# Kernel tuning notes

Hardware: AMD Instinct MI355X
Metric: run time of the kernel (lower is better)

## Reference

```python
import jax, jax.numpy as jnp
import numpy as np

BN_EPS = 1e-5

def _square_distance(src, dst):
    # src: (B,N,3), dst: (B,S,3) -> (B,N,S)
    d = -2.0 * jnp.einsum('bnc,bsc->bns', src, dst)
    d = d + jnp.sum(src * src, -1)[:, :, None]
    d = d + jnp.sum(dst * dst, -1)[:, None, :]
    return d

def _bn_relu(x, gamma, beta):
    # x: (B,N,C); training-mode batchnorm over (B,N)
    mean = jnp.mean(x, axis=(0, 1))
    var = jnp.mean(jnp.square(x - mean), axis=(0, 1))
    y = (x - mean) * jax.lax.rsqrt(var + BN_EPS) * gamma + beta
    return jax.nn.relu(y)

def setup_inputs() -> dict:
    key = jax.random.key(0)
    ks = jax.random.split(key, 12)
    B, N, S, D1, D2 = 8, 8192, 2048, 128, 256
    in_ch, mlp = 384, [256, 256]
    inp = {
        'xyz1': jax.random.normal(ks[0], (B, 3, N), jnp.float32),
        'xyz2': jax.random.normal(ks[1], (B, 3, S), jnp.float32),
        'points1': jax.random.normal(ks[2], (B, D1, N), jnp.float32),
        'points2': jax.random.normal(ks[3], (B, D2, S), jnp.float32),
    }
    last = in_ch
    for i, out in enumerate(mlp):
        inp[f'W{i+1}'] = jax.random.normal(ks[4 + 2 * i], (out, last), jnp.float32) * (1.0 / np.sqrt(last))
        inp[f'b{i+1}'] = jnp.zeros((out,), jnp.float32)
        inp[f'g{i+1}'] = jnp.ones((out,), jnp.float32)
        inp[f'beta{i+1}'] = jnp.zeros((out,), jnp.float32)
        last = out
    return inp

def reference(xyz1, xyz2, points1, points2, W1, b1, g1, beta1, W2, b2, g2, beta2):
    p1 = jnp.transpose(xyz1, (0, 2, 1))   # (B,N,3)
    p2 = jnp.transpose(xyz2, (0, 2, 1))   # (B,S,3)
    f2 = jnp.transpose(points2, (0, 2, 1))  # (B,S,D2)

    dists = _square_distance(p1, p2)      # (B,N,S)
    neg_d, idx = jax.lax.top_k(-dists, 3)  # 3 smallest distances
    d3 = -neg_d                            # (B,N,3)
    dist_recip = 1.0 / (d3 + 1e-8)
    weight = dist_recip / jnp.sum(dist_recip, axis=2, keepdims=True)  # (B,N,3)

    gathered = jax.vmap(lambda p, i: p[i])(f2, idx)   # (B,N,3,D2)
    interp = jnp.sum(gathered * weight[..., None], axis=2)  # (B,N,D2)

    f1 = jnp.transpose(points1, (0, 2, 1))  # (B,N,D1)
    x = jnp.concatenate([f1, interp], axis=-1)  # (B,N,D1+D2)

    x = _bn_relu(jnp.einsum('bnc,oc->bno', x, W1) + b1, g1, beta1)
    x = _bn_relu(jnp.einsum('bnc,oc->bno', x, W2) + b2, g2, beta2)
    return jnp.transpose(x, (0, 2, 1))  # (B,256,N)
```

## Files before the change

### kernel.cpp

```cpp
#include <hip/hip_runtime.h>

#define B_   8
#define N_   8192
#define S_   2048
#define D1_  128
#define D2_  256
#define O_   256
#define BN_  (B_*N_)

typedef __bf16 bf16;
typedef __bf16 bf16x8_t __attribute__((ext_vector_type(8)));
typedef __bf16 bf16x4_t __attribute__((ext_vector_type(4)));
typedef float  f32x4_t  __attribute__((ext_vector_type(4)));

static const size_t OFF_IDX  = 0;
static const size_t OFF_W    = 786432;
static const size_t OFF_PRT  = 393216;
static const size_t OFF_XP   = 1572864;
static const size_t OFF_Z    = 51904512;
static const size_t OFF_SS1  = 85458944;
static const size_t OFF_SS2  = 85460992;

#define GL16(gsrc, ldst) \
  __builtin_amdgcn_global_load_lds((const __attribute__((address_space(1))) void*)(gsrc), \
                                   (__attribute__((address_space(3))) void*)(ldst), 16, 0, 0)

__global__ __launch_bounds__(256) void k_prep(const float* __restrict__ p1, bf16* __restrict__ xp,
                                              const float* __restrict__ p2, bf16* __restrict__ f2t) {
  __shared__ float lds[64][65];
  const int bid = blockIdx.x;
  const int t = threadIdx.x;
  if (bid < 1024) {
    const int g  = bid * 256 + t;
    const int n4 = g & 2047;
    const int c8 = (g >> 11) & 15;
    const int b  = g >> 15;
    const int n  = n4 * 4;
    const float* src = p1 + ((size_t)b * D1_ + c8 * 8) * N_ + n;
    bf16x8_t o0, o1, o2, o3;
    #pragma unroll
    for (int j = 0; j < 8; ++j) {
      float4 v = *(const float4*)(src + (size_t)j * N_);
      o0[j] = (bf16)v.x; o1[j] = (bf16)v.y; o2[j] = (bf16)v.z; o3[j] = (bf16)v.w;
    }
    bf16* dst = xp + (((size_t)b * 48 + c8) * N_ + n) * 8;
    *(bf16x8_t*)(dst)      = o0;
    *(bf16x8_t*)(dst + 8)  = o1;
    *(bf16x8_t*)(dst + 16) = o2;
    *(bf16x8_t*)(dst + 24) = o3;
  } else {
    const int bid2 = bid - 1024;
    const int b = bid2 & 7;
    const int inner = bid2 >> 3;
    const int s0 = (inner & 31) * 64;
    const int c0 = (inner >> 5) * 64;
    {
      const int cr = t >> 2, scb = (t & 3) * 16;
      const float* src = p2 + ((size_t)b * D2_ + c0 + cr) * S_ + s0 + scb;
      #pragma unroll
      for (int i = 0; i < 4; ++i) {
        const float4 v = *(const float4*)(src + 4 * i);
        lds[cr][scb + 4 * i + 0] = v.x; lds[cr][scb + 4 * i + 1] = v.y;
        lds[cr][scb + 4 * i + 2] = v.z; lds[cr][scb + 4 * i + 3] = v.w;
      }
    }
    __syncthreads();
    const int co = (t & 7) * 8;
    #pragma unroll
    for (int pass = 0; pass < 2; ++pass) {
      const int s = pass * 32 + (t >> 3);
      bf16x8_t o;
      #pragma unroll
      for (int j = 0; j < 8; ++j) o[j] = (bf16)lds[co + j][s];
      *(bf16x8_t*)(f2t + ((size_t)b * S_ + s0 + s) * D2_ + c0 + co) = o;
    }
  }
}

__device__ __forceinline__ void ins3(float d, int i,
                                     float& d0, float& d1, float& d2,
                                     int& i0, int& i1, int& i2) {
  const bool c2 = d < d2, c1 = d < d1, c0 = d < d0;
  const float nd2 = c1 ? d1 : (c2 ? d : d2); const int ni2 = c1 ? i1 : (c2 ? i : i2);
  const float nd1 = c0 ? d0 : (c1 ? d : d1); const int ni1 = c0 ? i0 : (c1 ? i : i1);
  d0 = c0 ? d : d0; i0 = c0 ? i : i0;
  d1 = nd1; i1 = ni1; d2 = nd2; i2 = ni2;
}

__global__ __launch_bounds__(256) void k_nn3(const float* __restrict__ xyz1, const float* __restrict__ xyz2,
                                             int* __restrict__ idxw, float* __restrict__ www) {
  __shared__ float4 sq[4][S_ / 4];
  __shared__ float  pd[4][64][3];
  __shared__ int    pi[4][64][3];
  const int tid  = threadIdx.x;
  const int lane = tid & 63, w = tid >> 6;
  const int b     = blockIdx.y;
  const int nbase = blockIdx.x * 64;

  const float* x2 = xyz2 + (size_t)b * 3 * S_;
  for (int j = tid; j < S_ / 4; j += 256) {
    const float4 x = *(const float4*)(x2 + 4 * j);
    const float4 y = *(const float4*)(x2 + S_ + 4 * j);
    const float4 z = *(const float4*)(x2 + 2 * S_ + 4 * j);
    float4 qq;
    qq.x = fmaf(x.x, x.x, fmaf(y.x, y.x, z.x * z.x));
    qq.y = fmaf(x.y, x.y, fmaf(y.y, y.y, z.y * z.y));
    qq.z = fmaf(x.z, x.z, fmaf(y.z, y.z, z.z * z.z));
    qq.w = fmaf(x.w, x.w, fmaf(y.w, y.w, z.w * z.w));
    sq[0][j] = x; sq[1][j] = y; sq[2][j] = z; sq[3][j] = qq;
  }

  const int n = nbase + lane;
  const float* x1 = xyz1 + (size_t)b * 3 * N_;
  const float px = x1[n], py = x1[N_ + n], pz = x1[2 * N_ + n];
  const float ax = -2.f * px, ay = -2.f * py, az = -2.f * pz;
  __syncthreads();

  float e0 = 3.4e38f, e1 = 3.4e38f, e2 = 3.4e38f;
  int   i0 = 0, i1 = 0, i2 = 0;

  const int jb = w * (S_ / 16);
  #pragma unroll 2
  for (int j = jb; j < jb + S_ / 16; ++j) {
    const float4 qx = sq[0][j], qy = sq[1][j], qz = sq[2][j], qq = sq[3][j];
    #define CAND(C, SI)                                                        \
      {                                                                        \
        const float E = fmaf(ax, qx.C, fmaf(ay, qy.C, fmaf(az, qz.C, qq.C))); \
        if (__any(E < e2)) {                                                   \
          const bool l0 = E < e0, l1 = E < e1, l2 = E < e2;                    \
          const int ni1 = l0 ? i0 : (l1 ? (SI) : i1);                          \
          const int ni2 = l1 ? i1 : (l2 ? (SI) : i2);                          \
          i0 = l0 ? (SI) : i0; i1 = ni1; i2 = ni2;                             \
          const float ne1 = __builtin_amdgcn_fmed3f(E, e0, e1);                \
          const float ne2 = __builtin_amdgcn_fmed3f(E, e1, e2);                \
          e0 = fminf(E, e0); e1 = ne1; e2 = ne2;                               \
        }                                                                      \
      }
    CAND(x, 4 * j + 0)
    CAND(y, 4 * j + 1)
    CAND(z, 4 * j + 2)
    CAND(w, 4 * j + 3)
    #undef CAND
  }

  const float pp = fmaf(px, px, fmaf(py, py, pz * pz));
  pd[w][lane][0] = e0 + pp; pd[w][lane][1] = e1 + pp; pd[w][lane][2] = e2 + pp;
  pi[w][lane][0] = i0; pi[w][lane][1] = i1; pi[w][lane][2] = i2;
  __syncthreads();

  if (tid < 64) {
    float d0 = pd[0][tid][0], d1 = pd[0][tid][1], d2 = pd[0][tid][2];
    int   j0 = pi[0][tid][0], j1 = pi[0][tid][1], j2 = pi[0][tid][2];
    #pragma unroll
    for (int ck = 1; ck < 4; ++ck)
      #pragma unroll
      for (int k = 0; k < 3; ++k)
        ins3(pd[ck][tid][k], pi[ck][tid][k], d0, d1, d2, j0, j1, j2);
    const float r0 = 1.f / (d0 + 1e-8f), r1 = 1.f / (d1 + 1e-8f), r2 = 1.f / (d2 + 1e-8f);
    const float inv = 1.f / (r0 + r1 + r2);
    const int bn = b * N_ + nbase + tid;
    idxw[bn] = j0; idxw[BN_ + bn] = j1; idxw[2 * BN_ + bn] = j2;
    www[bn] = r0 * inv; www[BN_ + bn] = r1 * inv; www[2 * BN_ + bn] = r2 * inv;
  }
}

__global__ __launch_bounds__(256) void k_interp(const bf16* __restrict__ f2t, const int* __restrict__ idxw,
                                                const float* __restrict__ www, bf16* __restrict__ xp) {
  const int bid = blockIdx.x;
  const int b = bid & 7;
  const int n = (bid >> 3) * 8 + (threadIdx.x & 7);
  const int c8 = threadIdx.x >> 3;
  const int bn = b * N_ + n;
  const int j0 = idxw[bn], j1 = idxw[BN_ + bn], j2 = idxw[2 * BN_ + bn];
  const float w0 = www[bn], w1 = www[BN_ + bn], w2 = www[2 * BN_ + bn];
  const bf16* base = f2t + (size_t)b * S_ * D2_ + c8 * 8;
  const bf16x8_t v0 = *(const bf16x8_t*)(base + (size_t)j0 * D2_);
  const bf16x8_t v1 = *(const bf16x8_t*)(base + (size_t)j1 * D2_);
  const bf16x8_t v2 = *(const bf16x8_t*)(base + (size_t)j2 * D2_);
  bf16x8_t out;
  #pragma unroll
  for (int j = 0; j < 8; ++j)
    out[j] = (bf16)(w0 * (float)v0[j] + w1 * (float)v1[j] + w2 * (float)v2[j]);
  *(bf16x8_t*)(xp + (((size_t)b * 48 + 16 + c8) * N_ + (size_t)n) * 8) = out;
}

__global__ __launch_bounds__(256) void k_wprep(const float* __restrict__ W1, const float* __restrict__ W2,
                                               bf16* __restrict__ img) {
  const int g = blockIdx.x * 256 + threadIdx.x;
  if (g < 12288) {
    const int e = g * 8;
    const int imgblk = e >> 12, r = e & 4095;
    const int kc = r >> 10, row = (r & 1023) >> 3;
    const int mblk = imgblk / 12, kt32 = imgblk % 12;
    const float* s = W1 + (size_t)(mblk * 128 + row) * 384 + kt32 * 32 + kc * 8;
    const float4 f0 = *(const float4*)(s), f1 = *(const float4*)(s + 4);
    bf16x8_t h;
    h[0] = (bf16)f0.x; h[1] = (bf16)f0.y; h[2] = (bf16)f0.z; h[3] = (bf16)f0.w;
    h[4] = (bf16)f1.x; h[5] = (bf16)f1.y; h[6] = (bf16)f1.z; h[7] = (bf16)f1.w;
    *(bf16x8_t*)(img + e) = h;
  } else if (g < 20480) {
    const int e = (g - 12288) * 8;
    const int imgblk = e >> 12, r = e & 4095;
    const int kc = r >> 10, row = (r & 1023) >> 3;
    const int mblk = imgblk >> 3, kt32 = imgblk & 7;
    const float* s = W2 + (size_t)(mblk * 128 + row) * 256 + kt32 * 32 + kc * 8;
    const float4 f0 = *(const float4*)(s), f1 = *(const float4*)(s + 4);
    bf16x8_t h;
    h[0] = (bf16)f0.x; h[1] = (bf16)f0.y; h[2] = (bf16)f0.z; h[3] = (bf16)f0.w;
    h[4] = (bf16)f1.x; h[5] = (bf16)f1.y; h[6] = (bf16)f1.z; h[7] = (bf16)f1.w;
    *(bf16x8_t*)(img + 98304 + e) = h;
  }
}

template<int K>
__global__ __launch_bounds__(256) void k_gemm(const bf16* __restrict__ Wimg, const float* __restrict__ bias,
                                              const bf16* __restrict__ X, bf16* __restrict__ Zp,
                                              float* __restrict__ part) {
  __shared__ bf16 As[4096];
  __shared__ bf16 Bt[4096];
  __shared__ float stl[2][128][2];
  const int tid = threadIdx.x;
  const int lane = tid & 63, wid = tid >> 6;
  const int wr = wid >> 1, wc = wid & 1;
  const int dd = blockIdx.x;
  const int xcd = dd & 7, pos = dd >> 3;
  const int b = pos >> 4, q = pos & 15;
  const int m0 = (q & 1) * 128;
  const int ncol = xcd * 8 + (q >> 1);
  const int n0 = ncol * 128;
  const int mblk = m0 >> 7;
  const int l15 = lane & 15, l4 = lane >> 4;

  f32x4_t acc[4][4];
  #pragma unroll
  for (int i = 0; i < 4; ++i)
    #pragma unroll
    for (int j = 0; j < 4; ++j) { f32x4_t z = {0.f, 0.f, 0.f, 0.f}; acc[i][j] = z; }

  const bf16* Xb = X + (size_t)b * (K / 8) * ((size_t)N_ * 8);

  for (int kt = 0; kt < K; kt += 32) {
    const bf16* asrc = Wimg + (size_t)(mblk * (K / 32) + (kt >> 5)) * 4096 + wid * 1024 + lane * 8;
    GL16(asrc,       &As[wid * 1024]);
    GL16(asrc + 512, &As[wid * 1024 + 512]);
    const bf16* bsrc = Xb + ((size_t)(kt >> 3) + wid) * ((size_t)N_ * 8) + ((size_t)n0 + lane) * 8;
    GL16(bsrc,       &Bt[wid * 1024]);
    GL16(bsrc + 512, &Bt[wid * 1024 + 512]);
    __syncthreads();
    bf16x8_t af[4], bfr[4];
    #pragma unroll
    for (int mi = 0; mi < 4; ++mi) af[mi]  = *(const bf16x8_t*)&As[l4 * 1024 + (wr * 64 + mi * 16 + l15) * 8];
    #pragma unroll
    for (int ni = 0; ni < 4; ++ni) bfr[ni] = *(const bf16x8_t*)&Bt[l4 * 1024 + (wc * 64 + ni * 16 + l15) * 8];
    #pragma unroll
    for (int mi = 0; mi < 4; ++mi)
      #pragma unroll
      for (int ni = 0; ni < 4; ++ni)
        acc[mi][ni] = __builtin_amdgcn_mfma_f32_16x16x32_bf16(af[mi], bfr[ni], acc[mi][ni], 0, 0, 0);
    __syncthreads();
  }
  bf16* Zb = Zp + (size_t)b * 32 * ((size_t)N_ * 8);
  #pragma unroll
  for (int mi = 0; mi < 4; ++mi) {
    const int obase = m0 + wr * 64 + mi * 16 + l4 * 4;
    const float4 bv = *(const float4*)(bias + obase);
    const size_t gofs = (size_t)(obase >> 3) * ((size_t)N_ * 8) + (obase & 7);
    float sv0 = 0.f, sv1 = 0.f, sv2 = 0.f, sv3 = 0.f;
    float qv0 = 0.f, qv1 = 0.f, qv2 = 0.f, qv3 = 0.f;
    #pragma unroll
    for (int ni = 0; ni < 4; ++ni) {
      const int nn = n0 + wc * 64 + ni * 16 + l15;
      const float v0 = acc[mi][ni][0] + bv.x;
      const float v1 = acc[mi][ni][1] + bv.y;
      const float v2 = acc[mi][ni][2] + bv.z;
      const float v3 = acc[mi][ni][3] + bv.w;
      bf16x4_t o;
      o[0] = (bf16)v0; o[1] = (bf16)v1; o[2] = (bf16)v2; o[3] = (bf16)v3;
      *(bf16x4_t*)(Zb + gofs + (size_t)nn * 8) = o;
      sv0 += v0; qv0 = fmaf(v0, v0, qv0);
      sv1 += v1; qv1 = fmaf(v1, v1, qv1);
      sv2 += v2; qv2 = fmaf(v2, v2, qv2);
      sv3 += v3; qv3 = fmaf(v3, v3, qv3);
    }
    #pragma unroll
    for (int off = 1; off < 16; off <<= 1) {
      sv0 += __shfl_xor(sv0, off); qv0 += __shfl_xor(qv0, off);
      sv1 += __shfl_xor(sv1, off); qv1 += __shfl_xor(qv1, off);
      sv2 += __shfl_xor(sv2, off); qv2 += __shfl_xor(qv2, off);
      sv3 += __shfl_xor(sv3, off); qv3 += __shfl_xor(qv3, off);
    }
    if (l15 == 0) {
      const int ol = wr * 64 + mi * 16 + l4 * 4;
      stl[wc][ol + 0][0] = sv0; stl[wc][ol + 0][1] = qv0;
      stl[wc][ol + 1][0] = sv1; stl[wc][ol + 1][1] = qv1;
      stl[wc][ol + 2][0] = sv2; stl[wc][ol + 2][1] = qv2;
      stl[wc][ol + 3][0] = sv3; stl[wc][ol + 3][1] = qv3;
    }
  }
  __syncthreads();
  if (tid < 128) {
    const float s  = stl[0][tid][0] + stl[1][tid][0];
    const float sq = stl[0][tid][1] + stl[1][tid][1];
    const int ib = b * 64 + ncol;
    part[(size_t)(m0 + tid) * 512 + ib]       = s;
    part[(size_t)(256 + m0 + tid) * 512 + ib] = sq;
  }
}

__global__ __launch_bounds__(256) void k_gemm2f(const bf16* __restrict__ Wimg, const float* __restrict__ bias,
                                                const bf16* __restrict__ Z1, const float* __restrict__ ss,
                                                bf16* __restrict__ Zp, float* __restrict__ part) {
  __shared__ bf16 As[4096];
  __shared__ bf16 Bt[4096];
  __shared__ float stl[2][128][2];
  __shared__ float ssl[512];
  const int tid = threadIdx.x;
  const int lane = tid & 63, wid = tid >> 6;
  const int wr = wid >> 1, wc = wid & 1;
  const int dd = blockIdx.x;
  const int xcd = dd & 7, pos = dd >> 3;
  const int b = pos >> 4, q = pos & 15;
  const int m0 = (q & 1) * 128;
  const int ncol = xcd * 8 + (q >> 1);
  const int n0 = ncol * 128;
  const int mblk = m0 >> 7;
  const int l15 = lane & 15, l4 = lane >> 4;

  ssl[tid] = ss[tid]; ssl[256 + tid] = ss[256 + tid];

  f32x4_t acc[4][4];
  #pragma unroll
  for (int i = 0; i < 4; ++i)
    #pragma unroll
    for (int j = 0; j < 4; ++j) { f32x4_t z = {0.f, 0.f, 0.f, 0.f}; acc[i][j] = z; }

  const bf16* Z1b = Z1 + (size_t)b * 32 * ((size_t)N_ * 8);
  __syncthreads();

  for (int kt = 0; kt < 256; kt += 32) {
    const bf16* asrc = Wimg + (size_t)(mblk * 8 + (kt >> 5)) * 4096 + wid * 1024 + lane * 8;
    GL16(asrc,       &As[wid * 1024]);
    GL16(asrc + 512, &As[wid * 1024 + 512]);
    const int kc8 = (kt >> 3) + wid;
    const bf16* bsrc = Z1b + (size_t)kc8 * ((size_t)N_ * 8) + ((size_t)n0 + lane) * 8;
    const bf16x8_t rb0 = *(const bf16x8_t*)(bsrc);
    const bf16x8_t rb1 = *(const bf16x8_t*)(bsrc + 512);
    const int cb = kc8 * 8;
    bf16x8_t ob0, ob1;
    #pragma unroll
    for (int j = 0; j < 8; ++j) {
      const float sc = ssl[cb + j], sh = ssl[256 + cb + j];
      ob0[j] = (bf16)fmaxf(fmaf((float)rb0[j], sc, sh), 0.f);
      ob1[j] = (bf16)fmaxf(fmaf((float)rb1[j], sc, sh), 0.f);
    }
    *(bf16x8_t*)&Bt[wid * 1024 + lane * 8]       = ob0;
    *(bf16x8_t*)&Bt[wid * 1024 + 512 + lane * 8] = ob1;
    __syncthreads();
    bf16x8_t af[4], bfr[4];
    #pragma unroll
    for (int mi = 0; mi < 4; ++mi) af[mi]  = *(const bf16x8_t*)&As[l4 * 1024 + (wr * 64 + mi * 16 + l15) * 8];
    #pragma unroll
    for (int ni = 0; ni < 4; ++ni) bfr[ni] = *(const bf16x8_t*)&Bt[l4 * 1024 + (wc * 64 + ni * 16 + l15) * 8];
    #pragma unroll
    for (int mi = 0; mi < 4; ++mi)
      #pragma unroll
      for (int ni = 0; ni < 4; ++ni)
        acc[mi][ni] = __builtin_amdgcn_mfma_f32_16x16x32_bf16(af[mi], bfr[ni], acc[mi][ni], 0, 0, 0);
    __syncthreads();
  }
  bf16* Zb = Zp + (size_t)b * 32 * ((size_t)N_ * 8);
  #pragma unroll
  for (int mi = 0; mi < 4; ++mi) {
    const int obase = m0 + wr * 64 + mi * 16 + l4 * 4;
    const float4 bv = *(const float4*)(bias + obase);
    const size_t gofs = (size_t)(obase >> 3) * ((size_t)N_ * 8) + (obase & 7);
    float sv0 = 0.f, sv1 = 0.f, sv2 = 0.f, sv3 = 0.f;
    float qv0 = 0.f, qv1 = 0.f, qv2 = 0.f, qv3 = 0.f;
    #pragma unroll
    for (int ni = 0; ni < 4; ++ni) {
      const int nn = n0 + wc * 64 + ni * 16 + l15;
      const float v0 = acc[mi][ni][0] + bv.x;
      const float v1 = acc[mi][ni][1] + bv.y;
      const float v2 = acc[mi][ni][2] + bv.z;
      const float v3 = acc[mi][ni][3] + bv.w;
      bf16x4_t o;
      o[0] = (bf16)v0; o[1] = (bf16)v1; o[2] = (bf16)v2; o[3] = (bf16)v3;
      *(bf16x4_t*)(Zb + gofs + (size_t)nn * 8) = o;
      sv0 += v0; qv0 = fmaf(v0, v0, qv0);
      sv1 += v1; qv1 = fmaf(v1, v1, qv1);
      sv2 += v2; qv2 = fmaf(v2, v2, qv2);
      sv3 += v3; qv3 = fmaf(v3, v3, qv3);
    }
    #pragma unroll
    for (int off = 1; off < 16; off <<= 1) {
      sv0 += __shfl_xor(sv0, off); qv0 += __shfl_xor(qv0, off);
      sv1 += __shfl_xor(sv1, off); qv1 += __shfl_xor(qv1, off);
      sv2 += __shfl_xor(sv2, off); qv2 += __shfl_xor(qv2, off);
      sv3 += __shfl_xor(sv3, off); qv3 += __shfl_xor(qv3, off);
    }
    if (l15 == 0) {
      const int ol = wr * 64 + mi * 16 + l4 * 4;
      stl[wc][ol + 0][0] = sv0; stl[wc][ol + 0][1] = qv0;
      stl[wc][ol + 1][0] = sv1; stl[wc][ol + 1][1] = qv1;
      stl[wc][ol + 2][0] = sv2; stl[wc][ol + 2][1] = qv2;
      stl[wc][ol + 3][0] = sv3; stl[wc][ol + 3][1] = qv3;
    }
  }
  __syncthreads();
  if (tid < 128) {
    const float s  = stl[0][tid][0] + stl[1][tid][0];
    const float sq = stl[0][tid][1] + stl[1][tid][1];
    const int ib = b * 64 + ncol;
    part[(size_t)(m0 + tid) * 512 + ib]       = s;
    part[(size_t)(256 + m0 + tid) * 512 + ib] = sq;
  }
}

__global__ __launch_bounds__(256) void k_ss(const float* __restrict__ part, const float* __restrict__ g,
                                            const float* __restrict__ be, float* __restrict__ ss) {
  const int c = blockIdx.x, t = threadIdx.x;
  float s  = part[(size_t)c * 512 + t]         + part[(size_t)c * 512 + t + 256];
  float qv = part[(size_t)(256 + c) * 512 + t] + part[(size_t)(256 + c) * 512 + t + 256];
  #pragma unroll
  for (int off = 32; off; off >>= 1) { s += __shfl_down(s, off); qv += __shfl_down(qv, off); }
  __shared__ float r[8];
  const int w = t >> 6;
  if ((t & 63) == 0) { r[w] = s; r[4 + w] = qv; }
  __syncthreads();
  if (t == 0) {
    s  = r[0] + r[1] + r[2] + r[3];
    qv = r[4] + r[5] + r[6] + r[7];
    const float mean = s * (1.f / 65536.f);
    const float var  = qv * (1.f / 65536.f) - mean * mean;
    const float rstd = rsqrtf(var + 1e-5f);
    const float sc = g[c] * rstd;
    ss[c] = sc; ss[O_ + c] = be[c] - mean * sc;
  }
}

__global__ __launch_bounds__(256) void k_final_p(const bf16* __restrict__ Z, const float* __restrict__ ss,
                                                 float* __restrict__ Y) {
  const int b  = blockIdx.x >> 7;
  const int n0 = (blockIdx.x & 127) * 64;
  const int og = threadIdx.x >> 3, ns = threadIdx.x & 7;
  const bf16* src = Z + (((size_t)b * 32 + og) * N_ + n0 + ns * 8) * 8;
  bf16x8_t v[8];
  #pragma unroll
  for (int i = 0; i < 8; ++i) v[i] = *(const bf16x8_t*)(src + i * 8);
  float sc[8], sh[8];
  #pragma unroll
  for (int j = 0; j < 8; ++j) { sc[j] = ss[og * 8 + j]; sh[j] = ss[O_ + og * 8 + j]; }
  float* dst = Y + ((size_t)b * O_ + og * 8) * N_ + n0 + ns * 8;
  #pragma unroll
  for (int j = 0; j < 8; ++j) {
    float4 a0, a1;
    a0.x = fmaxf(fmaf((float)v[0][j], sc[j], sh[j]), 0.f);
    a0.y = fmaxf(fmaf((float)v[1][j], sc[j], sh[j]), 0.f);
    a0.z = fmaxf(fmaf((float)v[2][j], sc[j], sh[j]), 0.f);
    a0.w = fmaxf(fmaf((float)v[3][j], sc[j], sh[j]), 0.f);
    a1.x = fmaxf(fmaf((float)v[4][j], sc[j], sh[j]), 0.f);
    a1.y = fmaxf(fmaf((float)v[5][j], sc[j], sh[j]), 0.f);
    a1.z = fmaxf(fmaf((float)v[6][j], sc[j], sh[j]), 0.f);
    a1.w = fmaxf(fmaf((float)v[7][j], sc[j], sh[j]), 0.f);
    *(float4*)(dst + (size_t)j * N_)     = a0;
    *(float4*)(dst + (size_t)j * N_ + 4) = a1;
  }
}

extern "C" void kernel_launch(void* const* d_in, const int* in_sizes, int n_in,
                              void* d_out, int out_size, void* d_ws, size_t ws_size,
                              hipStream_t stream) {
  const float* xyz1    = (const float*)d_in[0];
  const float* xyz2    = (const float*)d_in[1];
  const float* points1 = (const float*)d_in[2];
  const float* points2 = (const float*)d_in[3];
  const float* W1  = (const float*)d_in[4];
  const float* b1  = (const float*)d_in[5];
  const float* g1  = (const float*)d_in[6];
  const float* be1 = (const float*)d_in[7];
  const float* W2  = (const float*)d_in[8];
  const float* b2  = (const float*)d_in[9];
  const float* g2  = (const float*)d_in[10];
  const float* be2 = (const float*)d_in[11];
  float* Y = (float*)d_out;
  char*  ws = (char*)d_ws;
  int*   idxw  = (int*)(ws + OFF_IDX);
  float* www   = (float*)(ws + OFF_W);
  bf16*  wimg1 = (bf16*)(ws + OFF_IDX);
  bf16*  wimg2 = wimg1 + 98304;
  float* part  = (float*)(ws + OFF_PRT);
  bf16*  xp    = (bf16*)(ws + OFF_XP);
  bf16*  z1    = (bf16*)(ws + OFF_Z);
  bf16*  f2t   = (bf16*)(ws + OFF_Z);
  bf16*  z2    = (bf16*)(ws + OFF_XP);
  float* ss1   = (float*)(ws + OFF_SS1);
  float* ss2   = (float*)(ws + OFF_SS2);

  hipLaunchKernelGGL(k_prep, dim3(2048), dim3(256), 0, stream, points1, xp, points2, f2t);
  hipLaunchKernelGGL(k_nn3, dim3(128, 8), dim3(256), 0, stream, xyz1, xyz2, idxw, www);
  hipLaunchKernelGGL(k_interp, dim3(8192), dim3(256), 0, stream, f2t, idxw, www, xp);
  hipLaunchKernelGGL(k_wprep, dim3(80), dim3(256), 0, stream, W1, W2, wimg1);
  hipLaunchKernelGGL((k_gemm<384>), dim3(1024), dim3(256), 0, stream, wimg1, b1, xp, z1, part);
  hipLaunchKernelGGL(k_ss, dim3(256), dim3(256), 0, stream, part, g1, be1, ss1);
  hipLaunchKernelGGL(k_gemm2f, dim3(1024), dim3(256), 0, stream, wimg2, b2, z1, ss1, z2, part);
  hipLaunchKernelGGL(k_ss, dim3(256), dim3(256), 0, stream, part, g2, be2, ss2);
  hipLaunchKernelGGL(k_final_p, dim3(1024), dim3(256), 0, stream, z2, ss2, Y);
}
```

Baseline: 163.5 us.

## Fuse nearest-neighbor search and input prep into one interleaved kernel launch

Merges the memory-bound prep kernel (bf16 repacking of points1 and transpose of points2) with the compute-bound 3-NN search kernel into a single launch of 3072 blocks. Every third block runs the NN search and the remaining blocks do prep work, so ALU-heavy and bandwidth-heavy work can share CUs concurrently. This also removes one launch boundary. In exchange, all blocks reserve the larger shared-memory footprint, which may reduce occupancy for the prep blocks.

```diff
diff --git a/kernel.cpp b/kernel.cpp
--- a/kernel.cpp
+++ b/kernel.cpp
@@ -25,142 +25,142 @@
   __builtin_amdgcn_global_load_lds((const __attribute__((address_space(1))) void*)(gsrc), \
                                    (__attribute__((address_space(3))) void*)(ldst), 16, 0, 0)
 
-__global__ __launch_bounds__(256) void k_prep(const float* __restrict__ p1, bf16* __restrict__ xp,
+__global__ __launch_bounds__(256) void k_nn3p(const float* __restrict__ xyz1, const float* __restrict__ xyz2,
+                                              int* __restrict__ idxw, float* __restrict__ www,
+                                              const float* __restrict__ p1, bf16* __restrict__ xp,
                                               const float* __restrict__ p2, bf16* __restrict__ f2t) {
-  __shared__ float lds[64][65];
-  const int bid = blockIdx.x;
+  __shared__ __align__(16) char raw[38912];
+  const int g = blockIdx.x;
   const int t = threadIdx.x;
-  if (bid < 1024) {
-    const int g  = bid * 256 + t;
-    const int n4 = g & 2047;
-    const int c8 = (g >> 11) & 15;
-    const int b  = g >> 15;
-    const int n  = n4 * 4;
-    const float* src = p1 + ((size_t)b * D1_ + c8 * 8) * N_ + n;
-    bf16x8_t o0, o1, o2, o3;
-    #pragma unroll
-    for (int j = 0; j < 8; ++j) {
-      float4 v = *(const float4*)(src + (size_t)j * N_);
-      o0[j] = (bf16)v.x; o1[j] = (bf16)v.y; o2[j] = (bf16)v.z; o3[j] = (bf16)v.w;
-    }
-    bf16* dst = xp + (((size_t)b * 48 + c8) * N_ + n) * 8;
-    *(bf16x8_t*)(dst)      = o0;
-    *(bf16x8_t*)(dst + 8)  = o1;
-    *(bf16x8_t*)(dst + 16) = o2;
-    *(bf16x8_t*)(dst + 24) = o3;
+
+  if (g % 3 == 0) {
+    float4 (*sq)[512]    = (float4(*)[512])raw;
+    float  (*pd)[64][3]  = (float(*)[64][3])(raw + 32768);
+    int    (*pi)[64][3]  = (int(*)[64][3])(raw + 35840);
+    const int nid  = g / 3;
+    const int lane = t & 63, w = t >> 6;
+    const int b     = nid >> 7;
+    const int nbase = (nid & 127) * 64;
+
+    const float* x2 = xyz2 + (size_t)b * 3 * S_;
+    for (int j = t; j < S_ / 4; j += 256) {
+      const float4 x = *(const float4*)(x2 + 4 * j);
+      const float4 y = *(const float4*)(x2 + S_ + 4 * j);
+      const float4 z = *(const float4*)(x2 + 2 * S_ + 4 * j);
+      float4 qq;
+      qq.x = fmaf(x.x, x.x, fmaf(y.x, y.x, z.x * z.x));
+      qq.y = fmaf(x.y, x.y, fmaf(y.y, y.y, z.y * z.y));
+      qq.z = fmaf(x.z, x.z, fmaf(y.z, y.z, z.z * z.z));
+      qq.w = fmaf(x.w, x.w, fmaf(y.w, y.w, z.w * z.w));
+      sq[0][j] = x; sq[1][j] = y; sq[2][j] = z; sq[3][j] = qq;
+    }
+
+    const int n = nbase + lane;
+    const float* x1 = xyz1 + (size_t)b * 3 * N_;
+    const float px = x1[n], py = x1[N_ + n], pz = x1[2 * N_ + n];
+    const float ax = -2.f * px, ay = -2.f * py, az = -2.f * pz;
+    __syncthreads();
+
+    float e0 = 3.4e38f, e1 = 3.4e38f, e2 = 3.4e38f;
+    int   i0 = 0, i1 = 0, i2 = 0;
+
+    const int jb = w * (S_ / 16);
+    #pragma unroll 2
+    for (int j = jb; j < jb + S_ / 16; ++j) {
+      const float4 qx = sq[0][j], qy = sq[1][j], qz = sq[2][j], qq = sq[3][j];
+      #define CAND(C, SI)                                                        \
+        {                                                                        \
+          const float E = fmaf(ax, qx.C, fmaf(ay, qy.C, fmaf(az, qz.C, qq.C))); \
+          if (__any(E < e2)) {                                                   \
+            const bool l0 = E < e0, l1 = E < e1, l2 = E < e2;                    \
+            const int ni1 = l0 ? i0 : (l1 ? (SI) : i1);                          \
+            const int ni2 = l1 ? i1 : (l2 ? (SI) : i2);                          \
+            i0 = l0 ? (SI) : i0; i1 = ni1; i2 = ni2;                             \
+            const float ne1 = __builtin_amdgcn_fmed3f(E, e0, e1);                \
+            const float ne2 = __builtin_amdgcn_fmed3f(E, e1, e2);                \
+            e0 = fminf(E, e0); e1 = ne1; e2 = ne2;                               \
+          }                                                                      \
+        }
+      CAND(x, 4 * j + 0)
+      CAND(y, 4 * j + 1)
+      CAND(z, 4 * j + 2)
+      CAND(w, 4 * j + 3)
+      #undef CAND
+    }
+
+    const float pp = fmaf(px, px, fmaf(py, py, pz * pz));
+    pd[w][lane][0] = e0 + pp; pd[w][lane][1] = e1 + pp; pd[w][lane][2] = e2 + pp;
+    pi[w][lane][0] = i0; pi[w][lane][1] = i1; pi[w][lane][2] = i2;
+    __syncthreads();
+
+    if (t < 64) {
+      float d0 = pd[0][t][0], d1 = pd[0][t][1], d2 = pd[0][t][2];
+      int   j0 = pi[0][t][0], j1 = pi[0][t][1], j2 = pi[0][t][2];
+      #pragma unroll
+      for (int ck = 1; ck < 4; ++ck)
+        #pragma unroll
+        for (int k = 0; k < 3; ++k) {
+          const float dv = pd[ck][t][k]; const int iv = pi[ck][t][k];
+          const bool c2 = dv < d2, c1 = dv < d1, c0 = dv < d0;
+          const float nd2 = c1 ? d1 : (c2 ? dv : d2); const int ni2 = c1 ? j1 : (c2 ? iv : j2);
+          const float nd1 = c0 ? d0 : (c1 ? dv : d1); const int ni1 = c0 ? j0 : (c1 ? iv : j1);
+          d0 = c0 ? dv : d0; j0 = c0 ? iv : j0;
+          d1 = nd1; j1 = ni1; d2 = nd2; j2 = ni2;
+        }
+      const float r0 = 1.f / (d0 + 1e-8f), r1 = 1.f / (d1 + 1e-8f), r2 = 1.f / (d2 + 1e-8f);
+      const float inv = 1.f / (r0 + r1 + r2);
+      const int bn = b * N_ + nbase + t;
+      idxw[bn] = j0; idxw[BN_ + bn] = j1; idxw[2 * BN_ + bn] = j2;
+      www[bn] = r0 * inv; www[BN_ + bn] = r1 * inv; www[2 * BN_ + bn] = r2 * inv;
+    }
   } else {
-    const int bid2 = bid - 1024;
-    const int b = bid2 & 7;
-    const int inner = bid2 >> 3;
-    const int s0 = (inner & 31) * 64;
-    const int c0 = (inner >> 5) * 64;
-    {
-      const int cr = t >> 2, scb = (t & 3) * 16;
-      const float* src = p2 + ((size_t)b * D2_ + c0 + cr) * S_ + s0 + scb;
+    const int p = g - g / 3 - 1;
+    if (p < 1024) {
+      const int gg = p * 256 + t;
+      const int n4 = gg & 2047;
+      const int c8 = (gg >> 11) & 15;
+      const int b  = gg >> 15;
+      const int n  = n4 * 4;
+      const float* src = p1 + ((size_t)b * D1_ + c8 * 8) * N_ + n;
+      bf16x8_t o0, o1, o2, o3;
       #pragma unroll
-      for (int i = 0; i < 4; ++i) {
-        const float4 v = *(const float4*)(src + 4 * i);
-        lds[cr][scb + 4 * i + 0] = v.x; lds[cr][scb + 4 * i + 1] = v.y;
-        lds[cr][scb + 4 * i + 2] = v.z; lds[cr][scb + 4 * i + 3] = v.w;
+      for (int j = 0; j < 8; ++j) {
+        float4 v = *(const float4*)(src + (size_t)j * N_);
+        o0[j] = (bf16)v.x; o1[j] = (bf16)v.y; o2[j] = (bf16)v.z; o3[j] = (bf16)v.w;
       }
-    }
-    __syncthreads();
-    const int co = (t & 7) * 8;
-    #pragma unroll
-    for (int pass = 0; pass < 2; ++pass) {
-      const int s = pass * 32 + (t >> 3);
-      bf16x8_t o;
+      bf16* dst = xp + (((size_t)b * 48 + c8) * N_ + n) * 8;
+      *(bf16x8_t*)(dst)      = o0;
+      *(bf16x8_t*)(dst + 8)  = o1;
+      *(bf16x8_t*)(dst + 16) = o2;
+      *(bf16x8_t*)(dst + 24) = o3;
+    } else {
+      float (*lds)[65] = (float(*)[65])raw;
+      const int bid2 = p - 1024;
+      const int b = bid2 & 7;
+      const int inner = bid2 >> 3;
+      const int s0 = (inner & 31) * 64;
+      const int c0 = (inner >> 5) * 64;
+      {
+        const int cr = t >> 2, scb = (t & 3) * 16;
+        const float* src = p2 + ((size_t)b * D2_ + c0 + cr) * S_ + s0 + scb;
+        #pragma unroll
+        for (int i = 0; i < 4; ++i) {
+          const float4 v = *(const float4*)(src + 4 * i);
+          lds[cr][scb + 4 * i + 0] = v.x; lds[cr][scb + 4 * i + 1] = v.y;
+          lds[cr][scb + 4 * i + 2] = v.z; lds[cr][scb + 4 * i + 3] = v.w;
+        }
+      }
+      __syncthreads();
+      const int co = (t & 7) * 8;
       #pragma unroll
-      for (int j = 0; j < 8; ++j) o[j] = (bf16)lds[co + j][s];
-      *(bf16x8_t*)(f2t + ((size_t)b * S_ + s0 + s) * D2_ + c0 + co) = o;
-    }
-  }
-}
-
-__device__ __forceinline__ void ins3(float d, int i,
-                                     float& d0, float& d1, float& d2,
-                                     int& i0, int& i1, int& i2) {
-  const bool c2 = d < d2, c1 = d < d1, c0 = d < d0;
-  const float nd2 = c1 ? d1 : (c2 ? d : d2); const int ni2 = c1 ? i1 : (c2 ? i : i2);
-  const float nd1 = c0 ? d0 : (c1 ? d : d1); const int ni1 = c0 ? i0 : (c1 ? i : i1);
-  d0 = c0 ? d : d0; i0 = c0 ? i : i0;
-  d1 = nd1; i1 = ni1; d2 = nd2; i2 = ni2;
-}
-
-__global__ __launch_bounds__(256) void k_nn3(const float* __restrict__ xyz1, const float* __restrict__ xyz2,
-                                             int* __restrict__ idxw, float* __restrict__ www) {
-  __shared__ float4 sq[4][S_ / 4];
-  __shared__ float  pd[4][64][3];
-  __shared__ int    pi[4][64][3];
-  const int tid  = threadIdx.x;
-  const int lane = tid & 63, w = tid >> 6;
-  const int b     = blockIdx.y;
-  const int nbase = blockIdx.x * 64;
-
-  const float* x2 = xyz2 + (size_t)b * 3 * S_;
-  for (int j = tid; j < S_ / 4; j += 256) {
-    const float4 x = *(const float4*)(x2 + 4 * j);
-    const float4 y = *(const float4*)(x2 + S_ + 4 * j);
-    const float4 z = *(const float4*)(x2 + 2 * S_ + 4 * j);
-    float4 qq;
-    qq.x = fmaf(x.x, x.x, fmaf(y.x, y.x, z.x * z.x));
-    qq.y = fmaf(x.y, x.y, fmaf(y.y, y.y, z.y * z.y));
-    qq.z = fmaf(x.z, x.z, fmaf(y.z, y.z, z.z * z.z));
-    qq.w = fmaf(x.w, x.w, fmaf(y.w, y.w, z.w * z.w));
-    sq[0][j] = x; sq[1][j] = y; sq[2][j] = z; sq[3][j] = qq;
-  }
-
-  const int n = nbase + lane;
-  const float* x1 = xyz1 + (size_t)b * 3 * N_;
-  const float px = x1[n], py = x1[N_ + n], pz = x1[2 * N_ + n];
-  const float ax = -2.f * px, ay = -2.f * py, az = -2.f * pz;
-  __syncthreads();
-
-  float e0 = 3.4e38f, e1 = 3.4e38f, e2 = 3.4e38f;
-  int   i0 = 0, i1 = 0, i2 = 0;
-
-  const int jb = w * (S_ / 16);
-  #pragma unroll 2
-  for (int j = jb; j < jb + S_ / 16; ++j) {
-    const float4 qx = sq[0][j], qy = sq[1][j], qz = sq[2][j], qq = sq[3][j];
-    #define CAND(C, SI)                                                        \
-      {                                                                        \
-        const float E = fmaf(ax, qx.C, fmaf(ay, qy.C, fmaf(az, qz.C, qq.C))); \
-        if (__any(E < e2)) {                                                   \
-          const bool l0 = E < e0, l1 = E < e1, l2 = E < e2;                    \
-          const int ni1 = l0 ? i0 : (l1 ? (SI) : i1);                          \
-          const int ni2 = l1 ? i1 : (l2 ? (SI) : i2);                          \
-          i0 = l0 ? (SI) : i0; i1 = ni1; i2 = ni2;                             \
-          const float ne1 = __builtin_amdgcn_fmed3f(E, e0, e1);                \
-          const float ne2 = __builtin_amdgcn_fmed3f(E, e1, e2);                \
-          e0 = fminf(E, e0); e1 = ne1; e2 = ne2;                               \
-        }                                                                      \
+      for (int pass = 0; pass < 2; ++pass) {
+        const int s = pass * 32 + (t >> 3);
+        bf16x8_t o;
+        #pragma unroll
+        for (int j = 0; j < 8; ++j) o[j] = (bf16)lds[co + j][s];
+        *(bf16x8_t*)(f2t + ((size_t)b * S_ + s0 + s) * D2_ + c0 + co) = o;
       }
-    CAND(x, 4 * j + 0)
-    CAND(y, 4 * j + 1)
-    CAND(z, 4 * j + 2)
-    CAND(w, 4 * j + 3)
-    #undef CAND
-  }
-
-  const float pp = fmaf(px, px, fmaf(py, py, pz * pz));
-  pd[w][lane][0] = e0 + pp; pd[w][lane][1] = e1 + pp; pd[w][lane][2] = e2 + pp;
-  pi[w][lane][0] = i0; pi[w][lane][1] = i1; pi[w][lane][2] = i2;
-  __syncthreads();
-
-  if (tid < 64) {
-    float d0 = pd[0][tid][0], d1 = pd[0][tid][1], d2 = pd[0][tid][2];
-    int   j0 = pi[0][tid][0], j1 = pi[0][tid][1], j2 = pi[0][tid][2];
-    #pragma unroll
-    for (int ck = 1; ck < 4; ++ck)
-      #pragma unroll
-      for (int k = 0; k < 3; ++k)
-        ins3(pd[ck][tid][k], pi[ck][tid][k], d0, d1, d2, j0, j1, j2);
-    const float r0 = 1.f / (d0 + 1e-8f), r1 = 1.f / (d1 + 1e-8f), r2 = 1.f / (d2 + 1e-8f);
-    const float inv = 1.f / (r0 + r1 + r2);
-    const int bn = b * N_ + nbase + tid;
-    idxw[bn] = j0; idxw[BN_ + bn] = j1; idxw[2 * BN_ + bn] = j2;
-    www[bn] = r0 * inv; www[BN_ + bn] = r1 * inv; www[2 * BN_ + bn] = r2 * inv;
+    }
   }
 }
 
@@ -496,8 +496,8 @@
   float* ss1   = (float*)(ws + OFF_SS1);
   float* ss2   = (float*)(ws + OFF_SS2);
 
-  hipLaunchKernelGGL(k_prep, dim3(2048), dim3(256), 0, stream, points1, xp, points2, f2t);
-  hipLaunchKernelGGL(k_nn3, dim3(128, 8), dim3(256), 0, stream, xyz1, xyz2, idxw, www);
+  hipLaunchKernelGGL(k_nn3p, dim3(3072), dim3(256), 0, stream,
+                     xyz1, xyz2, idxw, www, points1, xp, points2, f2t);
   hipLaunchKernelGGL(k_interp, dim3(8192), dim3(256), 0, stream, f2t, idxw, www, xp);
   hipLaunchKernelGGL(k_wprep, dim3(80), dim3(256), 0, stream, W1, W2, wimg1);
   hipLaunchKernelGGL((k_gemm<384>), dim3(1024), dim3(256), 0, stream, wimg1, b1, xp, z1, part);
```

Result: slower. 168.6 us (+3.1%).
